# Optimization experiments

Measured on AMD Instinct MI355X. Metric: run time of the kernel, lower is better.

The kernel has to match this reference:

```python
import jax, jax.numpy as jnp
import numpy as np

N = 100000   # nodes
E = 1000000  # edges per block
P = 100000   # pos/neg link edges
IN = 128
H = 64


def setup_inputs() -> dict:
    key = jax.random.key(0)
    ks = jax.random.split(key, 24)
    d = {}
    d["x"] = jax.random.normal(ks[0], (N, IN), jnp.float32)
    d["edge_weight"] = jax.random.uniform(ks[1], (3, E), jnp.float32)
    d["src"] = jax.random.randint(ks[2], (E,), 0, N)
    d["dst"] = jax.random.randint(ks[3], (E,), 0, N)
    d["pos_src"] = jax.random.randint(ks[4], (P,), 0, N)
    d["pos_dst"] = jax.random.randint(ks[5], (P,), 0, N)
    d["neg_src"] = jax.random.randint(ks[6], (P,), 0, N)
    d["neg_dst"] = jax.random.randint(ks[7], (P,), 0, N)
    s = 1.0 / np.sqrt(IN)
    h = 1.0 / np.sqrt(H)
    d["W0"] = jax.random.normal(ks[8], (IN, H), jnp.float32) * s
    d["b0"] = jnp.zeros((H,), jnp.float32)
    d["W1"] = jax.random.normal(ks[9], (H, H), jnp.float32) * h
    d["b1"] = jnp.zeros((H,), jnp.float32)
    d["W2"] = jax.random.normal(ks[10], (H, H), jnp.float32) * h
    d["b2"] = jnp.zeros((H,), jnp.float32)
    d["P0"] = jax.random.normal(ks[11], (H, H), jnp.float32) * h
    d["pb0"] = jnp.zeros((H,), jnp.float32)
    d["P1"] = jax.random.normal(ks[12], (H, H), jnp.float32) * h
    d["pb1"] = jnp.zeros((H,), jnp.float32)
    d["P2"] = jax.random.normal(ks[13], (H, 1), jnp.float32) * h
    d["pb2"] = jnp.zeros((1,), jnp.float32)
    return d


def _graph_conv(h, W, b, src, dst, ew, n_nodes):
    # DGL GraphConv, norm='both': D_out^{-1/2} on source feats,
    # edge-weighted sum aggregation, D_in^{-1/2} on result, then linear.
    ones = jnp.ones(src.shape[0], h.dtype)
    deg_out = jax.ops.segment_sum(ones, src, num_segments=n_nodes)
    deg_in = jax.ops.segment_sum(ones, dst, num_segments=n_nodes)
    norm_src = jax.lax.rsqrt(jnp.maximum(deg_out, 1.0))
    norm_dst = jax.lax.rsqrt(jnp.maximum(deg_in, 1.0))
    # apply weight before aggregation (in_feats >= out_feats); math-equivalent either way
    hw = (h * norm_src[:, None]) @ W            # [N, H]
    msg = hw[src] * ew[:, None]                 # [E, H] gather + scale
    agg = jax.ops.segment_sum(msg, dst, num_segments=n_nodes)  # scatter-add
    return agg * norm_dst[:, None] + b


def reference(x, edge_weight, src, dst, pos_src, pos_dst, neg_src, neg_dst,
              W0, b0, W1, b1, W2, b2, P0, pb0, P1, pb1, P2, pb2):
    h = jax.nn.relu(_graph_conv(x, W0, b0, src, dst, edge_weight[0], N))
    h = jax.nn.relu(_graph_conv(h, W1, b1, src, dst, edge_weight[1], N))
    h = _graph_conv(h, W2, b2, src, dst, edge_weight[2], N)  # no relu on last layer

    def mlp(z):
        z = jax.nn.relu(z @ P0 + pb0)
        z = jax.nn.relu(z @ P1 + pb1)
        return z @ P2 + pb2

    h_pos = mlp(h[pos_src] * h[pos_dst])  # [P, 1]
    h_neg = mlp(h[neg_src] * h[neg_dst])  # [P, 1]
    return (h_pos, h_neg)
```

## Files before the change

### kernel.cpp

```cpp
#include <hip/hip_runtime.h>


#define NN 100000
#define NE 1000000
#define NP 100000
#define SCAN_NB 98

__device__ __forceinline__ void row_fma(float4& acc, float xv, const float4& wv) {
    acc.x = fmaf(xv, wv.x, acc.x);
    acc.y = fmaf(xv, wv.y, acc.y);
    acc.z = fmaf(xv, wv.z, acc.z);
    acc.w = fmaf(xv, wv.w, acc.w);
}

__global__ void deg_kernel(const int* __restrict__ src, const int* __restrict__ dst,
                           int* __restrict__ deg_out, int* __restrict__ deg_in, int E) {
    int tid = blockIdx.x * blockDim.x + threadIdx.x;
    int stride = gridDim.x * blockDim.x;
    for (int e = tid; e < E; e += stride) {
        atomicAdd(&deg_out[src[e]], 1);
        atomicAdd(&deg_in[dst[e]], 1);
    }
}

__global__ void norm_kernel(const int* __restrict__ deg_out, const int* __restrict__ deg_in,
                            float* __restrict__ norm_src, float* __restrict__ norm_dst, int n) {
    int i = blockIdx.x * blockDim.x + threadIdx.x;
    if (i < n) {
        norm_src[i] = rsqrtf(fmaxf((float)deg_out[i], 1.0f));
        norm_dst[i] = rsqrtf(fmaxf((float)deg_in[i], 1.0f));
    }
}

__global__ __launch_bounds__(1024) void scan_block(const int* __restrict__ deg,
                                                   int* __restrict__ tmp_excl,
                                                   int* __restrict__ blocksums, int n) {
    __shared__ int wsums[16];
    const int i = blockIdx.x * 1024 + threadIdx.x;
    const int lane = threadIdx.x & 63, w = threadIdx.x >> 6;
    int v = (i < n) ? deg[i] : 0;
    int s = v;
#pragma unroll
    for (int off = 1; off < 64; off <<= 1) {
        int u = __shfl_up(s, off, 64);
        if (lane >= off) s += u;
    }
    if (lane == 63) wsums[w] = s;
    __syncthreads();
    if (w == 0) {
        int wv = (lane < 16) ? wsums[lane] : 0;
#pragma unroll
        for (int off = 1; off < 16; off <<= 1) {
            int u = __shfl_up(wv, off, 64);
            if (lane >= off) wv += u;
        }
        if (lane < 16) wsums[lane] = wv;
    }
    __syncthreads();
    int excl = s - v + (w > 0 ? wsums[w - 1] : 0);
    if (i < n) tmp_excl[i] = excl;
    if (threadIdx.x == 1023) blocksums[blockIdx.x] = excl + v;
}

__global__ void scan_sums(int* __restrict__ bs, int nb) {
    __shared__ int wtot[2];
    const int t = threadIdx.x;
    const int lane = t & 63, w = t >> 6;
    int v = (t < nb) ? bs[t] : 0;
    int s = v;
#pragma unroll
    for (int off = 1; off < 64; off <<= 1) {
        int u = __shfl_up(s, off, 64);
        if (lane >= off) s += u;
    }
    if (lane == 63) wtot[w] = s;
    __syncthreads();
    int excl = s - v + (w == 1 ? wtot[0] : 0);
    if (t < nb) bs[t] = excl;
}

__global__ __launch_bounds__(1024) void scan_apply(const int* __restrict__ tmp_excl,
                                                   const int* __restrict__ bs,
                                                   int* __restrict__ row_ptr,
                                                   int* __restrict__ cursor, int n) {
    const int i = blockIdx.x * 1024 + threadIdx.x;
    if (i < n) {
        int r = tmp_excl[i] + bs[blockIdx.x];
        row_ptr[i] = r;
        cursor[i] = r;
    }
    if (i == 0) row_ptr[n] = NE;
}

__global__ void csr_fill(const int* __restrict__ src, const int* __restrict__ dst,
                         const float* __restrict__ ew, int* __restrict__ cursor,
                         float4* __restrict__ cedge, int E) {
    int tid = blockIdx.x * blockDim.x + threadIdx.x;
    int stride = gridDim.x * blockDim.x;
    for (int e = tid; e < E; e += stride) {
        int d = dst[e];
        int slot = atomicAdd(&cursor[d], 1);
        float4 c;
        c.x = __int_as_float(src[e]);
        c.y = ew[e];
        c.z = ew[NE + e];
        c.w = ew[2 * NE + e];
        cedge[slot] = c;
    }
}

template <int WSEL, bool FINAL>
__global__ __launch_bounds__(256) void aggregate(const float* __restrict__ hw,
                                                 const float4* __restrict__ cedge,
                                                 const int* __restrict__ row_ptr,
                                                 const float* __restrict__ norm_src,
                                                 const float* __restrict__ norm_dst,
                                                 const float* __restrict__ bias,
                                                 float* __restrict__ outx, int n) {
    const int lane = threadIdx.x & 63;
    const int gw = (blockIdx.x * blockDim.x + threadIdx.x) >> 6;
    const int nw = (gridDim.x * blockDim.x) >> 6;
    const float blane = bias[lane];
    for (int node = gw; node < n; node += nw) {
        int beg = row_ptr[node], end = row_ptr[node + 1];
        float a0 = 0.f, a1 = 0.f;
        int i = beg;
        for (; i + 1 < end; i += 2) {
            float4 c0 = cedge[i], c1 = cedge[i + 1];
            int s0 = __float_as_int(c0.x), s1 = __float_as_int(c1.x);
            float w0 = (WSEL == 0) ? c0.y : (WSEL == 1) ? c0.z : c0.w;
            float w1 = (WSEL == 0) ? c1.y : (WSEL == 1) ? c1.z : c1.w;
            a0 = fmaf(hw[s0 * 64 + lane], w0, a0);
            a1 = fmaf(hw[s1 * 64 + lane], w1, a1);
        }
        if (i < end) {
            float4 c0 = cedge[i];
            int s0 = __float_as_int(c0.x);
            float w0 = (WSEL == 0) ? c0.y : (WSEL == 1) ? c0.z : c0.w;
            a0 = fmaf(hw[s0 * 64 + lane], w0, a0);
        }
        float a = a0 + a1;
        float nd = norm_dst[node];
        float t;
        if (FINAL) {
            t = fmaf(a, nd, blane);
        } else {
            t = fmaxf(fmaf(a, nd, blane), 0.f) * norm_src[node];
        }
        outx[node * 64 + lane] = t;
    }
}

template <int K, bool SCALE>
__global__ __launch_bounds__(256) void gemm_tile(const float* __restrict__ in,
                                                 const float* __restrict__ W,
                                                 const float* __restrict__ norm_src,
                                                 float* __restrict__ out, int n) {
    __shared__ float Xs[64][K + 4];
    __shared__ float Ws[K * 64];
    const int tid = threadIdx.x;
    for (int i = tid; i < K * 16; i += 256) ((float4*)Ws)[i] = ((const float4*)W)[i];
    __syncthreads();

    const int ntiles = (n + 63) >> 6;
    const int tr = tid >> 4, tc = tid & 15;

    for (int tile = blockIdx.x; tile < ntiles; tile += gridDim.x) {
        for (int idx = tid; idx < K * 16; idx += 256) {
            int r = idx / (K / 4), kq = idx % (K / 4);
            int row = tile * 64 + r;
            float4 v = make_float4(0.f, 0.f, 0.f, 0.f);
            if (row < n) v = *(const float4*)&in[row * K + kq * 4];
            *(float4*)&Xs[r][kq * 4] = v;
        }
        __syncthreads();

        float4 acc0 = {0, 0, 0, 0}, acc1 = {0, 0, 0, 0}, acc2 = {0, 0, 0, 0}, acc3 = {0, 0, 0, 0};
#pragma unroll 4
        for (int k4 = 0; k4 < K / 4; ++k4) {
            const int kb = k4 * 4;
            float4 xv0 = *(const float4*)&Xs[tr * 4 + 0][kb];
            float4 xv1 = *(const float4*)&Xs[tr * 4 + 1][kb];
            float4 xv2 = *(const float4*)&Xs[tr * 4 + 2][kb];
            float4 xv3 = *(const float4*)&Xs[tr * 4 + 3][kb];
            const float* wb = &Ws[kb * 64 + tc * 4];
            float4 wk;
            wk = *(const float4*)(wb);
            row_fma(acc0, xv0.x, wk); row_fma(acc1, xv1.x, wk); row_fma(acc2, xv2.x, wk); row_fma(acc3, xv3.x, wk);
            wk = *(const float4*)(wb + 64);
            row_fma(acc0, xv0.y, wk); row_fma(acc1, xv1.y, wk); row_fma(acc2, xv2.y, wk); row_fma(acc3, xv3.y, wk);
            wk = *(const float4*)(wb + 128);
            row_fma(acc0, xv0.z, wk); row_fma(acc1, xv1.z, wk); row_fma(acc2, xv2.z, wk); row_fma(acc3, xv3.z, wk);
            wk = *(const float4*)(wb + 192);
            row_fma(acc0, xv0.w, wk); row_fma(acc1, xv1.w, wk); row_fma(acc2, xv2.w, wk); row_fma(acc3, xv3.w, wk);
        }

#pragma unroll
        for (int i = 0; i < 4; ++i) {
            int row = tile * 64 + tr * 4 + i;
            if (row < n) {
                float4 o = (i == 0) ? acc0 : (i == 1) ? acc1 : (i == 2) ? acc2 : acc3;
                if (SCALE) {
                    float ns = norm_src[row];
                    o.x *= ns; o.y *= ns; o.z *= ns; o.w *= ns;
                }
                *(float4*)&out[row * 64 + tc * 4] = o;
            }
        }
        __syncthreads();
    }
}

#define ZST 76

__global__ __launch_bounds__(256) void mlp_tile(const float* __restrict__ hfin,
                                                const float* __restrict__ P0,
                                                const float* __restrict__ pb0,
                                                const float* __restrict__ P1,
                                                const float* __restrict__ pb1,
                                                const float* __restrict__ P2,
                                                const float* __restrict__ pb2,
                                                const int* __restrict__ pos_src,
                                                const int* __restrict__ pos_dst,
                                                const int* __restrict__ neg_src,
                                                const int* __restrict__ neg_dst,
                                                float* __restrict__ out, int P) {
    __shared__ float Zs[64][ZST];
    __shared__ float W0s[4096], W1s[4096];
    __shared__ float pb0s[64], pb1s[64], P2s[64];
    __shared__ int pas[64], pbs[64];
    const int tid = threadIdx.x;
    for (int i = tid; i < 1024; i += 256) {
        ((float4*)W0s)[i] = ((const float4*)P0)[i];
        ((float4*)W1s)[i] = ((const float4*)P1)[i];
    }
    if (tid < 64) {
        pb0s[tid] = pb0[tid];
        pb1s[tid] = pb1[tid];
        P2s[tid] = P2[tid];
    }
    const float pb2v = pb2[0];
    const int lane = tid & 63, w = tid >> 6;
    const int tr = tid >> 4, tc = tid & 15;
    const int ntiles = (2 * P) >> 6;

    for (int tile = blockIdx.x; tile < ntiles; tile += gridDim.x) {
        const int base = tile << 6;
        __syncthreads();
        if (tid < 64) {
            int p = base + tid;
            pas[tid] = (p < P) ? pos_src[p] : neg_src[p - P];
            pbs[tid] = (p < P) ? pos_dst[p] : neg_dst[p - P];
        }
        __syncthreads();

#pragma unroll 4
        for (int pi = w; pi < 64; pi += 4) {
            float ha = hfin[pas[pi] * 64 + lane];
            float hb = hfin[pbs[pi] * 64 + lane];
            Zs[pi][lane] = ha * hb;
        }
        __syncthreads();

        float4 acc0, acc1, acc2, acc3;
        {
            float4 binit = *(const float4*)&pb0s[tc * 4];
            acc0 = binit; acc1 = binit; acc2 = binit; acc3 = binit;
        }
#pragma unroll 4
        for (int k4 = 0; k4 < 16; ++k4) {
            const int kb = k4 * 4;
            float4 xv0 = *(const float4*)&Zs[tr * 4 + 0][kb];
            float4 xv1 = *(const float4*)&Zs[tr * 4 + 1][kb];
            float4 xv2 = *(const float4*)&Zs[tr * 4 + 2][kb];
            float4 xv3 = *(const float4*)&Zs[tr * 4 + 3][kb];
            const float* wb = &W0s[kb * 64 + tc * 4];
            float4 wk;
            wk = *(const float4*)(wb);
            row_fma(acc0, xv0.x, wk); row_fma(acc1, xv1.x, wk); row_fma(acc2, xv2.x, wk); row_fma(acc3, xv3.x, wk);
            wk = *(const float4*)(wb + 64);
            row_fma(acc0, xv0.y, wk); row_fma(acc1, xv1.y, wk); row_fma(acc2, xv2.y, wk); row_fma(acc3, xv3.y, wk);
            wk = *(const float4*)(wb + 128);
            row_fma(acc0, xv0.z, wk); row_fma(acc1, xv1.z, wk); row_fma(acc2, xv2.z, wk); row_fma(acc3, xv3.z, wk);
            wk = *(const float4*)(wb + 192);
            row_fma(acc0, xv0.w, wk); row_fma(acc1, xv1.w, wk); row_fma(acc2, xv2.w, wk); row_fma(acc3, xv3.w, wk);
        }
        __syncthreads();
#pragma unroll
        for (int i = 0; i < 4; ++i) {
            float4 o = (i == 0) ? acc0 : (i == 1) ? acc1 : (i == 2) ? acc2 : acc3;
            o.x = fmaxf(o.x, 0.f); o.y = fmaxf(o.y, 0.f); o.z = fmaxf(o.z, 0.f); o.w = fmaxf(o.w, 0.f);
            *(float4*)&Zs[tr * 4 + i][tc * 4] = o;
        }
        __syncthreads();

        {
            float4 binit = *(const float4*)&pb1s[tc * 4];
            acc0 = binit; acc1 = binit; acc2 = binit; acc3 = binit;
        }
#pragma unroll 4
        for (int k4 = 0; k4 < 16; ++k4) {
            const int kb = k4 * 4;
            float4 xv0 = *(const float4*)&Zs[tr * 4 + 0][kb];
            float4 xv1 = *(const float4*)&Zs[tr * 4 + 1][kb];
            float4 xv2 = *(const float4*)&Zs[tr * 4 + 2][kb];
            float4 xv3 = *(const float4*)&Zs[tr * 4 + 3][kb];
            const float* wb = &W1s[kb * 64 + tc * 4];
            float4 wk;
            wk = *(const float4*)(wb);
            row_fma(acc0, xv0.x, wk); row_fma(acc1, xv1.x, wk); row_fma(acc2, xv2.x, wk); row_fma(acc3, xv3.x, wk);
            wk = *(const float4*)(wb + 64);
            row_fma(acc0, xv0.y, wk); row_fma(acc1, xv1.y, wk); row_fma(acc2, xv2.y, wk); row_fma(acc3, xv3.y, wk);
            wk = *(const float4*)(wb + 128);
            row_fma(acc0, xv0.z, wk); row_fma(acc1, xv1.z, wk); row_fma(acc2, xv2.z, wk); row_fma(acc3, xv3.z, wk);
            wk = *(const float4*)(wb + 192);
            row_fma(acc0, xv0.w, wk); row_fma(acc1, xv1.w, wk); row_fma(acc2, xv2.w, wk); row_fma(acc3, xv3.w, wk);
        }
        __syncthreads();
#pragma unroll
        for (int i = 0; i < 4; ++i) {
            float4 o = (i == 0) ? acc0 : (i == 1) ? acc1 : (i == 2) ? acc2 : acc3;
            o.x = fmaxf(o.x, 0.f); o.y = fmaxf(o.y, 0.f); o.z = fmaxf(o.z, 0.f); o.w = fmaxf(o.w, 0.f);
            *(float4*)&Zs[tr * 4 + i][tc * 4] = o;
        }
        __syncthreads();

        {
            int p = tid >> 2, kq = tid & 3;
            float s = 0.f;
#pragma unroll
            for (int i = 0; i < 16; ++i) s = fmaf(Zs[p][kq * 16 + i], P2s[kq * 16 + i], s);
            s += __shfl_xor(s, 1, 64);
            s += __shfl_xor(s, 2, 64);
            if (kq == 0) out[base + p] = s + pb2v;
        }
    }
}

extern "C" void kernel_launch(void* const* d_in, const int* in_sizes, int n_in,
                              void* d_out, int out_size, void* d_ws, size_t ws_size,
                              hipStream_t stream) {
    const float* x     = (const float*)d_in[0];
    const float* ew    = (const float*)d_in[1];
    const int* src     = (const int*)d_in[2];
    const int* dst     = (const int*)d_in[3];
    const int* pos_src = (const int*)d_in[4];
    const int* pos_dst = (const int*)d_in[5];
    const int* neg_src = (const int*)d_in[6];
    const int* neg_dst = (const int*)d_in[7];
    const float* W0    = (const float*)d_in[8];
    const float* b0    = (const float*)d_in[9];
    const float* W1    = (const float*)d_in[10];
    const float* b1    = (const float*)d_in[11];
    const float* W2    = (const float*)d_in[12];
    const float* b2    = (const float*)d_in[13];
    const float* P0    = (const float*)d_in[14];
    const float* pb0   = (const float*)d_in[15];
    const float* P1    = (const float*)d_in[16];
    const float* pb1   = (const float*)d_in[17];
    const float* P2    = (const float*)d_in[18];
    const float* pb2   = (const float*)d_in[19];
    float* out = (float*)d_out;

    float* ws = (float*)d_ws;
    float* norm_src = ws;
    float* norm_dst = ws + 100000;
    int* cursor     = (int*)(ws + 200000);
    int* deg_in     = (int*)(ws + 300000);
    int* row_ptr    = (int*)(ws + 400000);
    float4* cedge   = (float4*)(ws + 500004);
    float* hw       = ws + 4500004;
    float* agg      = ws + 10900004;

    int* tmp_excl  = (int*)hw;
    int* blocksums = (int*)hw + NN;

    hipMemsetAsync(cursor, 0, 2 * NN * sizeof(int), stream);
    deg_kernel<<<2048, 256, 0, stream>>>(src, dst, cursor, deg_in, NE);
    norm_kernel<<<(NN + 255) / 256, 256, 0, stream>>>(cursor, deg_in, norm_src, norm_dst, NN);
    scan_block<<<SCAN_NB, 1024, 0, stream>>>(deg_in, tmp_excl, blocksums, NN);
    scan_sums<<<1, 128, 0, stream>>>(blocksums, SCAN_NB);
    scan_apply<<<SCAN_NB, 1024, 0, stream>>>(tmp_excl, blocksums, row_ptr, cursor, NN);
    csr_fill<<<2048, 256, 0, stream>>>(src, dst, ew, cursor, cedge, NE);

    const int NT = (NN + 63) / 64;

    gemm_tile<128, true><<<NT, 256, 0, stream>>>(x, W0, norm_src, hw, NN);
    aggregate<0, false><<<4096, 256, 0, stream>>>(hw, cedge, row_ptr, norm_src, norm_dst, b0, agg, NN);
    gemm_tile<64, false><<<NT, 256, 0, stream>>>(agg, W1, nullptr, hw, NN);
    aggregate<1, false><<<4096, 256, 0, stream>>>(hw, cedge, row_ptr, norm_src, norm_dst, b1, agg, NN);
    gemm_tile<64, false><<<NT, 256, 0, stream>>>(agg, W2, nullptr, hw, NN);
    aggregate<2, true><<<4096, 256, 0, stream>>>(hw, cedge, row_ptr, norm_src, norm_dst, b2, agg, NN);

    mlp_tile<<<1024, 256, 0, stream>>>(agg, P0, pb0, P1, pb1, P2, pb2,
                                       pos_src, pos_dst, neg_src, neg_dst, out, NP);
}
```

Before: 522.7 us.

## Vectorize degree counting, unroll aggregation by four, read weights from global

```diff
diff --git a/kernel.cpp b/kernel.cpp
--- a/kernel.cpp
+++ b/kernel.cpp
@@ -13,13 +13,19 @@
     acc.w = fmaf(xv, wv.w, acc.w);
 }
 
-__global__ void deg_kernel(const int* __restrict__ src, const int* __restrict__ dst,
-                           int* __restrict__ deg_out, int* __restrict__ deg_in, int E) {
+__global__ void deg_kernel(const int4* __restrict__ src4, const int4* __restrict__ dst4,
+                           int* __restrict__ deg_out, int* __restrict__ deg_in, int E4) {
     int tid = blockIdx.x * blockDim.x + threadIdx.x;
-    int stride = gridDim.x * blockDim.x;
-    for (int e = tid; e < E; e += stride) {
-        atomicAdd(&deg_out[src[e]], 1);
-        atomicAdd(&deg_in[dst[e]], 1);
+    if (tid < E4) {
+        int4 s = src4[tid], d = dst4[tid];
+        atomicAdd(&deg_out[s.x], 1);
+        atomicAdd(&deg_out[s.y], 1);
+        atomicAdd(&deg_out[s.z], 1);
+        atomicAdd(&deg_out[s.w], 1);
+        atomicAdd(&deg_in[d.x], 1);
+        atomicAdd(&deg_in[d.y], 1);
+        atomicAdd(&deg_in[d.z], 1);
+        atomicAdd(&deg_in[d.w], 1);
     }
 }
 
@@ -123,23 +129,28 @@
     const float blane = bias[lane];
     for (int node = gw; node < n; node += nw) {
         int beg = row_ptr[node], end = row_ptr[node + 1];
-        float a0 = 0.f, a1 = 0.f;
+        float a0 = 0.f, a1 = 0.f, a2 = 0.f, a3 = 0.f;
         int i = beg;
-        for (; i + 1 < end; i += 2) {
-            float4 c0 = cedge[i], c1 = cedge[i + 1];
+        for (; i + 3 < end; i += 4) {
+            float4 c0 = cedge[i], c1 = cedge[i + 1], c2 = cedge[i + 2], c3 = cedge[i + 3];
             int s0 = __float_as_int(c0.x), s1 = __float_as_int(c1.x);
+            int s2 = __float_as_int(c2.x), s3 = __float_as_int(c3.x);
             float w0 = (WSEL == 0) ? c0.y : (WSEL == 1) ? c0.z : c0.w;
             float w1 = (WSEL == 0) ? c1.y : (WSEL == 1) ? c1.z : c1.w;
+            float w2 = (WSEL == 0) ? c2.y : (WSEL == 1) ? c2.z : c2.w;
+            float w3 = (WSEL == 0) ? c3.y : (WSEL == 1) ? c3.z : c3.w;
             a0 = fmaf(hw[s0 * 64 + lane], w0, a0);
             a1 = fmaf(hw[s1 * 64 + lane], w1, a1);
-        }
-        if (i < end) {
+            a2 = fmaf(hw[s2 * 64 + lane], w2, a2);
+            a3 = fmaf(hw[s3 * 64 + lane], w3, a3);
+        }
+        for (; i < end; ++i) {
             float4 c0 = cedge[i];
             int s0 = __float_as_int(c0.x);
             float w0 = (WSEL == 0) ? c0.y : (WSEL == 1) ? c0.z : c0.w;
             a0 = fmaf(hw[s0 * 64 + lane], w0, a0);
         }
-        float a = a0 + a1;
+        float a = (a0 + a1) + (a2 + a3);
         float nd = norm_dst[node];
         float t;
         if (FINAL) {
@@ -157,11 +168,7 @@
                                                  const float* __restrict__ norm_src,
                                                  float* __restrict__ out, int n) {
     __shared__ float Xs[64][K + 4];
-    __shared__ float Ws[K * 64];
     const int tid = threadIdx.x;
-    for (int i = tid; i < K * 16; i += 256) ((float4*)Ws)[i] = ((const float4*)W)[i];
-    __syncthreads();
-
     const int ntiles = (n + 63) >> 6;
     const int tr = tid >> 4, tc = tid & 15;
 
@@ -183,7 +190,7 @@
             float4 xv1 = *(const float4*)&Xs[tr * 4 + 1][kb];
             float4 xv2 = *(const float4*)&Xs[tr * 4 + 2][kb];
             float4 xv3 = *(const float4*)&Xs[tr * 4 + 3][kb];
-            const float* wb = &Ws[kb * 64 + tc * 4];
+            const float* wb = &W[kb * 64 + tc * 4];
             float4 wk;
             wk = *(const float4*)(wb);
             row_fma(acc0, xv0.x, wk); row_fma(acc1, xv1.x, wk); row_fma(acc2, xv2.x, wk); row_fma(acc3, xv3.x, wk);
@@ -226,14 +233,9 @@
                                                 const int* __restrict__ neg_dst,
                                                 float* __restrict__ out, int P) {
     __shared__ float Zs[64][ZST];
-    __shared__ float W0s[4096], W1s[4096];
     __shared__ float pb0s[64], pb1s[64], P2s[64];
     __shared__ int pas[64], pbs[64];
     const int tid = threadIdx.x;
-    for (int i = tid; i < 1024; i += 256) {
-        ((float4*)W0s)[i] = ((const float4*)P0)[i];
-        ((float4*)W1s)[i] = ((const float4*)P1)[i];
-    }
     if (tid < 64) {
         pb0s[tid] = pb0[tid];
         pb1s[tid] = pb1[tid];
@@ -274,7 +276,7 @@
             float4 xv1 = *(const float4*)&Zs[tr * 4 + 1][kb];
             float4 xv2 = *(const float4*)&Zs[tr * 4 + 2][kb];
             float4 xv3 = *(const float4*)&Zs[tr * 4 + 3][kb];
-            const float* wb = &W0s[kb * 64 + tc * 4];
+            const float* wb = &P0[kb * 64 + tc * 4];
             float4 wk;
             wk = *(const float4*)(wb);
             row_fma(acc0, xv0.x, wk); row_fma(acc1, xv1.x, wk); row_fma(acc2, xv2.x, wk); row_fma(acc3, xv3.x, wk);
@@ -305,7 +307,7 @@
             float4 xv1 = *(const float4*)&Zs[tr * 4 + 1][kb];
             float4 xv2 = *(const float4*)&Zs[tr * 4 + 2][kb];
             float4 xv3 = *(const float4*)&Zs[tr * 4 + 3][kb];
-            const float* wb = &W1s[kb * 64 + tc * 4];
+            const float* wb = &P1[kb * 64 + tc * 4];
             float4 wk;
             wk = *(const float4*)(wb);
             row_fma(acc0, xv0.x, wk); row_fma(acc1, xv1.x, wk); row_fma(acc2, xv2.x, wk); row_fma(acc3, xv3.x, wk);
@@ -376,7 +378,8 @@
     int* blocksums = (int*)hw + NN;
 
     hipMemsetAsync(cursor, 0, 2 * NN * sizeof(int), stream);
-    deg_kernel<<<2048, 256, 0, stream>>>(src, dst, cursor, deg_in, NE);
+    deg_kernel<<<(NE / 4 + 255) / 256, 256, 0, stream>>>((const int4*)src, (const int4*)dst,
+                                                         cursor, deg_in, NE / 4);
     norm_kernel<<<(NN + 255) / 256, 256, 0, stream>>>(cursor, deg_in, norm_src, norm_dst, NN);
     scan_block<<<SCAN_NB, 1024, 0, stream>>>(deg_in, tmp_excl, blocksums, NN);
     scan_sums<<<1, 128, 0, stream>>>(blocksums, SCAN_NB);
```

Result: no change. 527.2 us (+0.9%).
